# Kernel tuning notes

Hardware: AMD Instinct MI355X
Metric: run time of the kernel (lower is better)

The kernel has to match this reference:

```python
import jax, jax.numpy as jnp
import numpy as np

N_HEAD = 16
N_KV = 4
HEAD_DIM = 128
EPS = float(np.finfo(np.float32).eps)  # torch F.rms_norm default eps


def _rope_tables(T, half, dtype=jnp.float32):
    inv_freq = 1.0 / (10000.0 ** (jnp.arange(half, dtype=dtype) / half))
    ang = jnp.arange(T, dtype=dtype)[:, None] * inv_freq[None, :]  # (T, half)
    cos = jnp.cos(ang)[None, :, None, :]  # (1, T, 1, half)
    sin = jnp.sin(ang)[None, :, None, :]
    return cos, sin


def setup_inputs() -> dict:
    key = jax.random.key(0)
    ks = jax.random.split(key, 5)
    B, T, C = 2, 2048, 2048
    x = jax.random.normal(ks[0], (B, T, C), dtype=jnp.float32)
    cos, sin = _rope_tables(T, HEAD_DIM // 2)
    s = 0.02
    W_Q = jax.random.normal(ks[1], (C, N_HEAD * HEAD_DIM), dtype=jnp.float32) * s
    W_K = jax.random.normal(ks[2], (C, N_KV * HEAD_DIM), dtype=jnp.float32) * s
    W_V = jax.random.normal(ks[3], (C, N_KV * HEAD_DIM), dtype=jnp.float32) * s
    W_O = jax.random.normal(ks[4], (C, C), dtype=jnp.float32) * s
    return {"x": x, "cos": cos, "sin": sin, "W_Q": W_Q, "W_K": W_K, "W_V": W_V, "W_O": W_O}


def _apply_rope(x, cos, sin):
    # x: (B,T,H,D); cos/sin: (1,T,1,D/2)
    d = x.shape[-1] // 2
    x1, x2 = x[..., :d], x[..., d:]
    return jnp.concatenate([x1 * cos + x2 * sin, -x1 * sin + x2 * cos], axis=-1)


def _rms_norm(x):
    return x * jax.lax.rsqrt(jnp.mean(x * x, axis=-1, keepdims=True) + EPS)


def reference(x, cos, sin, W_Q, W_K, W_V, W_O):
    B, T, C = x.shape
    G = N_HEAD // N_KV  # kv groups
    q = (x @ W_Q).reshape(B, T, N_HEAD, HEAD_DIM)
    k = (x @ W_K).reshape(B, T, N_KV, HEAD_DIM)
    v = (x @ W_V).reshape(B, T, N_KV, HEAD_DIM)
    q = _rms_norm(_apply_rope(q, cos[:, :T], sin[:, :T]))
    k = _rms_norm(_apply_rope(k, cos[:, :T], sin[:, :T]))
    # GQA: avoid materializing expanded K/V; group q by kv head
    qg = q.reshape(B, T, N_KV, G, HEAD_DIM)
    scale = 1.0 / jnp.sqrt(jnp.asarray(HEAD_DIM, dtype=x.dtype))
    scores = jnp.einsum("btkgd,bskd->bkgts", qg, k) * scale  # (B,Kv,G,T,T)
    causal = jnp.tril(jnp.ones((T, T), dtype=bool))
    scores = jnp.where(causal, scores, jnp.asarray(-jnp.inf, dtype=scores.dtype))
    attn = jax.nn.softmax(scores, axis=-1)
    out = jnp.einsum("bkgts,bskd->btkgd", attn, v).reshape(B, T, C)
    return out @ W_O
```

## Files before the change

kernel.cpp:

```cpp
#include <hip/hip_runtime.h>
#include <hip/hip_bf16.h>
#include <stdint.h>

typedef __bf16 bf16_4 __attribute__((ext_vector_type(4)));
typedef __bf16 bf16_8 __attribute__((ext_vector_type(8)));
typedef float f32x4 __attribute__((ext_vector_type(4)));

#define AS1 __attribute__((address_space(1)))
#define AS3 __attribute__((address_space(3)))

__device__ __forceinline__ void gload_lds16(const void* g, void* l) {
  __builtin_amdgcn_global_load_lds((const AS1 void*)g, (AS3 void*)l, 16, 0, 0);
}

__global__ void detect_dtype(const void* __restrict__ cosT, int* __restrict__ flag) {
  uint32_t w = *reinterpret_cast<const uint32_t*>(cosT);
  *flag = ((w & 0xFFFFu) == 0x3F80u) ? 1 : 0;
}

__global__ __launch_bounds__(256) void to_bf16_vec(const void* __restrict__ src,
                                                   __bf16* __restrict__ dst,
                                                   int n8, const int* __restrict__ flag) {
  const int i = blockIdx.x * 256 + threadIdx.x;
  if (i >= n8) return;
  if (*flag) {
    reinterpret_cast<int4*>(dst)[i] = reinterpret_cast<const int4*>(src)[i];
  } else {
    const float4* s = reinterpret_cast<const float4*>(src);
    const float4 a = s[2 * i], b = s[2 * i + 1];
    __bf16 o[8] = {(__bf16)a.x, (__bf16)a.y, (__bf16)a.z, (__bf16)a.w,
                   (__bf16)b.x, (__bf16)b.y, (__bf16)b.z, (__bf16)b.w};
    reinterpret_cast<int4*>(dst)[i] = *reinterpret_cast<int4*>(o);
  }
}

__global__ __launch_bounds__(256) void tables_to_f32(const void* __restrict__ c,
                                                     const void* __restrict__ s,
                                                     float* __restrict__ dst, int n,
                                                     const int* __restrict__ flag) {
  const int i = blockIdx.x * 256 + threadIdx.x;
  if (i >= n) return;
  if (*flag) {
    dst[i]     = (float)reinterpret_cast<const __bf16*>(c)[i];
    dst[n + i] = (float)reinterpret_cast<const __bf16*>(s)[i];
  } else {
    dst[i]     = reinterpret_cast<const float*>(c)[i];
    dst[n + i] = reinterpret_cast<const float*>(s)[i];
  }
}

__global__ void transpose_all(const void* __restrict__ WQ, const void* __restrict__ WK,
                              const void* __restrict__ WV, const void* __restrict__ WO,
                              __bf16* __restrict__ Wt, __bf16* __restrict__ WOt,
                              const int* __restrict__ flag) {
  __shared__ __bf16 t[32][33];
  const int bx = blockIdx.x;
  const void* src;
  __bf16* dst;
  int C, c0;
  if (bx < 64)      { src = WQ; dst = Wt;                          C = 2048; c0 = bx * 32; }
  else if (bx < 80) { src = WK; dst = Wt + (size_t)2048 * 2048;    C = 512;  c0 = (bx - 64) * 32; }
  else if (bx < 96) { src = WV; dst = Wt + (size_t)2560 * 2048;    C = 512;  c0 = (bx - 80) * 32; }
  else              { src = WO; dst = WOt;                         C = 2048; c0 = (bx - 96) * 32; }
  const int r0 = blockIdx.y * 32;
  const bool isb = (*flag != 0);
  #pragma unroll
  for (int i = 0; i < 32; i += 8) {
    const size_t idx = (size_t)(r0 + threadIdx.y + i) * C + c0 + threadIdx.x;
    t[threadIdx.y + i][threadIdx.x] =
        isb ? reinterpret_cast<const __bf16*>(src)[idx]
            : (__bf16)reinterpret_cast<const float*>(src)[idx];
  }
  __syncthreads();
  #pragma unroll
  for (int i = 0; i < 32; i += 8)
    dst[(size_t)(c0 + threadIdx.y + i) * 2048 + r0 + threadIdx.x] = t[threadIdx.x][threadIdx.y + i];
}

__global__ void vtrans(const __bf16* __restrict__ qkv, __bf16* __restrict__ vt) {
  __shared__ __bf16 t[32][33];
  const int b = blockIdx.z;
  const int t0 = blockIdx.x * 32, c0 = blockIdx.y * 32;
  #pragma unroll
  for (int i = 0; i < 32; i += 8)
    t[threadIdx.y + i][threadIdx.x] =
        qkv[(size_t)(b * 2048 + t0 + threadIdx.y + i) * 3072 + 2560 + c0 + threadIdx.x];
  __syncthreads();
  #pragma unroll
  for (int i = 0; i < 32; i += 8)
    vt[(size_t)(b * 512 + c0 + threadIdx.y + i) * 2048 + t0 + threadIdx.x] =
        t[threadIdx.x][threadIdx.y + i];
}

template <int DYN>
__global__ __launch_bounds__(512) void gemm8p(const __bf16* __restrict__ A,
                                              const __bf16* __restrict__ Bt,
                                              void* __restrict__ Cv,
                                              int M, int N, int K,
                                              const int* __restrict__ flag) {
  __shared__ __attribute__((aligned(16))) __bf16 As[2][128 * 64];
  __shared__ __attribute__((aligned(16))) __bf16 Bs[2][256 * 64];
  const int tid = threadIdx.x;
  const int lane = tid & 63, w = tid >> 6;
  const int wm = w >> 2, wn = w & 3;
  const int r = lane & 15, g = lane >> 4;
  const int bm = blockIdx.x * 128, bn = blockIdx.y * 256;
  const bool isb = DYN ? (*flag != 0) : true;
  const int NT = K >> 6;

  f32x4 acc[4][4] = {};

#define STA(kt, p, j)                                                              \
  {                                                                                \
    const int o_ = tid * 16 + (j) * 8192;                                          \
    const int row_ = o_ >> 7, blk_ = (o_ >> 4) & 7;                                \
    gload_lds16(A + (size_t)(bm + row_) * K + (kt) * 64 + ((blk_ ^ (row_ & 7)) << 3), \
                (char*)As[p] + o_);                                                \
  }
#define STB(kt, p, j)                                                              \
  {                                                                                \
    const int o_ = tid * 16 + (j) * 8192;                                          \
    const int rl_ = o_ >> 7, blk_ = (o_ >> 4) & 7;                                 \
    const int gr_ = ((rl_ >> 5) & 3) * 64 + ((rl_ >> 7) & 1) * 32 + (rl_ & 31);    \
    gload_lds16(Bt + (size_t)(bn + gr_) * K + (kt) * 64 + ((blk_ ^ (rl_ & 7)) << 3), \
                (char*)Bs[p] + o_);                                                \
  }

  STA(0, 0, 0); STA(0, 0, 1);
  STB(0, 0, 0); STB(0, 0, 1); STB(0, 0, 2); STB(0, 0, 3);
  asm volatile("s_waitcnt vmcnt(2)\ns_barrier" ::: "memory");

  for (int kt = 0; kt < NT; ++kt) {
    const int cur = kt & 1, nxt = cur ^ 1;
    const bool pf = (kt + 1 < NT);
    const char* Ac = (const char*)As[cur];
    const char* Bc = (const char*)Bs[cur];

    bf16_8 af[4][2], bf[2][2];
    #pragma unroll
    for (int m = 0; m < 4; ++m)
      #pragma unroll
      for (int kk = 0; kk < 2; ++kk) {
        const int row = wm * 64 + m * 16 + r;
        af[m][kk] = *reinterpret_cast<const bf16_8*>(
            Ac + row * 128 + (((kk * 4 + g) ^ (row & 7)) << 4));
      }
    #pragma unroll
    for (int n = 0; n < 2; ++n)
      #pragma unroll
      for (int kk = 0; kk < 2; ++kk) {
        const int rl = wn * 32 + n * 16 + r;
        bf[n][kk] = *reinterpret_cast<const bf16_8*>(
            Bc + rl * 128 + (((kk * 4 + g) ^ (rl & 7)) << 4));
      }
    if (pf) { STA(kt + 1, nxt, 0); STA(kt + 1, nxt, 1); STB(kt + 1, nxt, 0); }
    __builtin_amdgcn_s_barrier();
    __builtin_amdgcn_s_setprio(1);
    #pragma unroll
    for (int kk = 0; kk < 2; ++kk)
      #pragma unroll
      for (int m = 0; m < 4; ++m)
        #pragma unroll
        for (int n = 0; n < 2; ++n)
          acc[m][n] = __builtin_amdgcn_mfma_f32_16x16x32_bf16(af[m][kk], bf[n][kk], acc[m][n], 0, 0, 0);
    __builtin_amdgcn_s_setprio(0);
    if (pf) asm volatile("s_waitcnt vmcnt(3)\ns_barrier" ::: "memory");
    else    asm volatile("s_waitcnt vmcnt(0)\ns_barrier" ::: "memory");

    bf16_8 bg[2][2];
    #pragma unroll
    for (int n = 0; n < 2; ++n)
      #pragma unroll
      for (int kk = 0; kk < 2; ++kk) {
        const int rl = 128 + wn * 32 + n * 16 + r;
        bg[n][kk] = *reinterpret_cast<const bf16_8*>(
            Bc + rl * 128 + (((kk * 4 + g) ^ (rl & 7)) << 4));
      }
    if (pf) { STB(kt + 1, nxt, 1); STB(kt + 1, nxt, 2); STB(kt + 1, nxt, 3); }
    __builtin_amdgcn_s_barrier();
    __builtin_amdgcn_s_setprio(1);
    #pragma unroll
    for (int kk = 0; kk < 2; ++kk)
      #pragma unroll
      for (int m = 0; m < 4; ++m)
        #pragma unroll
        for (int n = 0; n < 2; ++n)
          acc[m][n + 2] = __builtin_amdgcn_mfma_f32_16x16x32_bf16(af[m][kk], bg[n][kk], acc[m][n + 2], 0, 0, 0);
    __builtin_amdgcn_s_setprio(0);
    if (pf) asm volatile("s_waitcnt vmcnt(2)\ns_barrier" ::: "memory");
    else    asm volatile("s_waitcnt vmcnt(0)\ns_barrier" ::: "memory");
  }
#undef STA
#undef STB

  #pragma unroll
  for (int m = 0; m < 4; ++m)
    #pragma unroll
    for (int n = 0; n < 4; ++n)
      #pragma unroll
      for (int j = 0; j < 4; ++j) {
        const int row = bm + wm * 64 + m * 16 + g * 4 + j;
        const int col = bn + wn * 64 + n * 16 + r;
        const float v = acc[m][n][j];
        if (isb) reinterpret_cast<__bf16*>(Cv)[(size_t)row * N + col] = (__bf16)v;
        else     reinterpret_cast<float*>(Cv)[(size_t)row * N + col] = v;
      }
}

__global__ __launch_bounds__(256) void rope_rms(__bf16* __restrict__ qkv,
                                                const float* __restrict__ csF) {
  const int gw = blockIdx.x * 4 + (threadIdx.x >> 6);
  const int lane = threadIdx.x & 63;
  const int head = gw % 20;
  const int m = gw / 20;
  const int t = m & 2047;
  __bf16* p = qkv + (size_t)m * 3072 + head * 128;
  const float x1 = (float)p[lane];
  const float x2 = (float)p[lane + 64];
  const float c = csF[t * 64 + lane];
  const float s = csF[131072 + t * 64 + lane];
  const float y1 = x1 * c + x2 * s;
  const float y2 = x2 * c - x1 * s;
  float ss = y1 * y1 + y2 * y2;
  #pragma unroll
  for (int mk = 32; mk >= 1; mk >>= 1) ss += __shfl_xor(ss, mk, 64);
  const float inv = rsqrtf(ss * (1.0f / 128.0f) + 1.1920929e-7f);
  p[lane] = (__bf16)(y1 * inv);
  p[lane + 64] = (__bf16)(y2 * inv);
}

__global__ __launch_bounds__(256) void attn_fwd4(const __bf16* __restrict__ qkv,
                                                 const __bf16* __restrict__ vt,
                                                 __bf16* __restrict__ out) {
  __shared__ __attribute__((aligned(16))) __bf16 Kl[2][64 * 128];
  __shared__ __attribute__((aligned(16))) __bf16 Vl[2][128 * 64];
  __shared__ __attribute__((aligned(16))) __bf16 Pl[4][16][72];

  const int tid = threadIdx.x, lane = tid & 63, w = tid >> 6;
  const int r = lane & 15, g = lane >> 4;
  const int lid = blockIdx.x;
  const int grp = lid & 7, inner = lid >> 3;
  const int b = grp >> 2, kvh = grp & 3;
  const int h = kvh * 4 + (inner & 3);
  const int x = inner >> 2;
  const int qtA = x, qtB = 31 - x;
  const int nA = qtA + 1, nB = qtB + 1;
  const __bf16* Kbase = qkv + (size_t)(b * 2048) * 3072 + 2048 + kvh * 128;
  const __bf16* Vbase = vt + (size_t)((b * 4 + kvh) * 128) * 2048;
  const float sc2 = 0.08838834764831845f * 1.44269504f;

#define STAGE(kt, p)                                                            \
  {                                                                             \
    _Pragma("unroll")                                                           \
    for (int i_ = 0; i_ < 4; ++i_) {                                            \
      const int o_ = tid * 16 + i_ * 4096;                                      \
      const int krow_ = o_ >> 8;                                                \
      const int jj_ = (o_ >> 4) & 15;                                           \
      const int gj_ = (jj_ & 8) | ((jj_ ^ krow_) & 7);                          \
      gload_lds16(Kbase + (size_t)((kt) * 64 + krow_) * 3072 + gj_ * 8,         \
                  (char*)Kl[p] + o_);                                           \
      const int d_ = o_ >> 7;                                                   \
      const int j2_ = (o_ >> 4) & 7;                                            \
      const int g2_ = j2_ ^ (d_ & 7);                                           \
      gload_lds16(Vbase + (size_t)d_ * 2048 + (kt) * 64 + g2_ * 8,              \
                  (char*)Vl[p] + o_);                                           \
    }                                                                           \
  }

#define TILE(qt_, qf_, acc_, mst_, lst_)                                        \
  do {                                                                          \
    f32x4 sacc[4] = {};                                                         \
    _Pragma("unroll")                                                           \
    for (int kb = 0; kb < 4; ++kb) {                                            \
      const int jj = kb * 4 + g;                                                \
      const int jp = (jj & 8) | ((jj ^ (r & 7)) & 7);                           \
      _Pragma("unroll")                                                         \
      for (int n = 0; n < 4; ++n) {                                             \
        const bf16_8 kf = *reinterpret_cast<const bf16_8*>(Kc + (n * 16 + r) * 256 + jp * 16); \
        sacc[n] = __builtin_amdgcn_mfma_f32_16x16x32_bf16(kf, qf_[kb], sacc[n], 0, 0, 0); \
      }                                                                         \
    }                                                                           \
    float p[4][4];                                                              \
    float pm = -1e30f;                                                          \
    _Pragma("unroll")                                                           \
    for (int n = 0; n < 4; ++n)                                                 \
      _Pragma("unroll")                                                         \
      for (int j = 0; j < 4; ++j) {                                             \
        float s = sacc[n][j] * sc2;                                             \
        p[n][j] = s;                                                            \
        pm = fmaxf(pm, s);                                                      \
      }                                                                         \
    if (kt == (qt_)) {                                                          \
      const int qpos_ = (qt_) * 64 + w * 16 + r;                                \
      pm = -1e30f;                                                              \
      _Pragma("unroll")                                                         \
      for (int n = 0; n < 4; ++n)                                               \
        _Pragma("unroll")                                                       \
        for (int j = 0; j < 4; ++j) {                                           \
          if (kt * 64 + n * 16 + g * 4 + j > qpos_) p[n][j] = -1e30f;           \
          pm = fmaxf(pm, p[n][j]);                                              \
        }                                                                       \
    }                                                                           \
    pm = fmaxf(pm, __shfl_xor(pm, 16, 64));                                     \
    pm = fmaxf(pm, __shfl_xor(pm, 32, 64));                                     \
    float mn = mst_;                                                            \
    if (!__all(pm - mst_ <= 12.0f)) {                                           \
      mn = fmaxf(mst_, pm);                                                     \
      const float alpha = exp2f(mst_ - mn);                                     \
      mst_ = mn;                                                                \
      lst_ *= alpha;                                                            \
      float av[4];                                                              \
      _Pragma("unroll")                                                         \
      for (int j = 0; j < 4; ++j) av[j] = __shfl(alpha, g * 4 + j, 64);         \
      _Pragma("unroll")                                                         \
      for (int dt = 0; dt < 8; ++dt)                                            \
        _Pragma("unroll")                                                       \
        for (int j = 0; j < 4; ++j) acc_[dt][j] *= av[j];                       \
    }                                                                           \
    float rs = 0.0f;                                                            \
    _Pragma("unroll")                                                           \
    for (int n = 0; n < 4; ++n)                                                 \
      _Pragma("unroll")                                                         \
      for (int j = 0; j < 4; ++j) {                                             \
        p[n][j] = exp2f(p[n][j] - mn);                                          \
        rs += p[n][j];                                                          \
      }                                                                         \
    rs += __shfl_xor(rs, 16, 64);                                               \
    rs += __shfl_xor(rs, 32, 64);                                               \
    lst_ += rs;                                                                 \
    _Pragma("unroll")                                                           \
    for (int n = 0; n < 4; ++n) {                                               \
      bf16_4 pk;                                                                \
      _Pragma("unroll")                                                         \
      for (int j = 0; j < 4; ++j) pk[j] = (__bf16)p[n][j];                      \
      *reinterpret_cast<bf16_4*>(&Pl[w][r][n * 16 + g * 4]) = pk;               \
    }                                                                           \
    _Pragma("unroll")                                                           \
    for (int half = 0; half < 2; ++half) {                                      \
      const bf16_8 pa = *reinterpret_cast<const bf16_8*>(&Pl[w][r][half * 32 + g * 8]); \
      _Pragma("unroll")                                                         \
      for (int dt = 0; dt < 8; ++dt) {                                          \
        const int d = dt * 16 + r;                                              \
        const bf16_8 vf = *reinterpret_cast<const bf16_8*>(Vc + d * 128 + ((half * 4 + g) ^ (d & 7)) * 16); \
        acc_[dt] = __builtin_amdgcn_mfma_f32_16x16x32_bf16(pa, vf, acc_[dt], 0, 0, 0); \
      }                                                                         \
    }                                                                           \
  } while (0)

  bf16_8 qfA[4], qfB[4];
  {
    const __bf16* qpA = qkv + (size_t)(b * 2048 + qtA * 64 + w * 16 + r) * 3072 + h * 128 + g * 8;
    const __bf16* qpB = qkv + (size_t)(b * 2048 + qtB * 64 + w * 16 + r) * 3072 + h * 128 + g * 8;
    #pragma unroll
    for (int kb = 0; kb < 4; ++kb) {
      qfA[kb] = *reinterpret_cast<const bf16_8*>(qpA + kb * 32);
      qfB[kb] = *reinterpret_cast<const bf16_8*>(qpB + kb * 32);
    }
  }

  f32x4 accA[8] = {}, accB[8] = {};
  float mstA = -1e30f, lstA = 0.0f, mstB = -1e30f, lstB = 0.0f;

  STAGE(0, 0);
  asm volatile("s_waitcnt vmcnt(0)" ::: "memory");
  __syncthreads();

  for (int kt = 0; kt < nB; ++kt) {
    const int cur = kt & 1;
    if (kt + 1 < nB) STAGE(kt + 1, cur ^ 1);
    const char* Kc = (const char*)Kl[cur];
    const char* Vc = (const char*)Vl[cur];

    if (kt < nA) TILE(qtA, qfA, accA, mstA, lstA);
    TILE(qtB, qfB, accB, mstB, lstB);

    asm volatile("s_waitcnt vmcnt(0)" ::: "memory");
    __syncthreads();
  }

  {
    float lv[4];
    #pragma unroll
    for (int j = 0; j < 4; ++j) lv[j] = 1.0f / __shfl(lstA, g * 4 + j, 64);
    #pragma unroll
    for (int dt = 0; dt < 8; ++dt)
      #pragma unroll
      for (int j = 0; j < 4; ++j) {
        const int t = qtA * 64 + w * 16 + g * 4 + j;
        out[(size_t)(b * 2048 + t) * 2048 + h * 128 + dt * 16 + r] = (__bf16)(accA[dt][j] * lv[j]);
      }
  }
  {
    float lv[4];
    #pragma unroll
    for (int j = 0; j < 4; ++j) lv[j] = 1.0f / __shfl(lstB, g * 4 + j, 64);
    #pragma unroll
    for (int dt = 0; dt < 8; ++dt)
      #pragma unroll
      for (int j = 0; j < 4; ++j) {
        const int t = qtB * 64 + w * 16 + g * 4 + j;
        out[(size_t)(b * 2048 + t) * 2048 + h * 128 + dt * 16 + r] = (__bf16)(accB[dt][j] * lv[j]);
      }
  }
#undef STAGE
#undef TILE
}

extern "C" void kernel_launch(void* const* d_in, const int* in_sizes, int n_in,
                              void* d_out, int out_size, void* d_ws, size_t ws_size,
                              hipStream_t stream) {
  const void* x    = d_in[0];
  const void* cosT = d_in[1];
  const void* sinT = d_in[2];
  const void* W_Q  = d_in[3];
  const void* W_K  = d_in[4];
  const void* W_V  = d_in[5];
  const void* W_O  = d_in[6];

  const int B = 2, T = 2048, C = 2048;
  const int M = B * T;
  const int NQKV = 3072;

  char* ws = (char*)d_ws;
  int*    flag = (int*)ws;                       ws += 256;
  float*  csF  = (float*)ws;                     ws += (size_t)2 * 131072 * 4;
  __bf16* xb   = (__bf16*)ws;                    ws += (size_t)M * C * 2;
  __bf16* Wt   = (__bf16*)ws;                    ws += (size_t)NQKV * C * 2;
  __bf16* WOt  = (__bf16*)ws;                    ws += (size_t)C * C * 2;
  __bf16* QKV  = (__bf16*)ws;                    ws += (size_t)M * NQKV * 2;
  __bf16* AO   = (__bf16*)ws;                    ws += (size_t)M * C * 2;
  __bf16* VT   = xb;

  detect_dtype<<<1, 1, 0, stream>>>(cosT, flag);
  tables_to_f32<<<131072 / 256, 256, 0, stream>>>(cosT, sinT, csF, 131072, flag);
  to_bf16_vec<<<(M * C / 8) / 256, 256, 0, stream>>>(x, xb, M * C / 8, flag);

  transpose_all<<<dim3(160, 64), dim3(32, 8), 0, stream>>>(W_Q, W_K, W_V, W_O, Wt, WOt, flag);

  gemm8p<0><<<dim3(M / 128, NQKV / 256), 512, 0, stream>>>(xb, Wt, QKV, M, NQKV, C, flag);
  rope_rms<<<dim3(M * 20 / 4), 256, 0, stream>>>(QKV, csF);
  vtrans<<<dim3(T / 32, 512 / 32, B), dim3(32, 8), 0, stream>>>(QKV, VT);
  attn_fwd4<<<dim3(512), 256, 0, stream>>>(QKV, VT, AO);
  gemm8p<1><<<dim3(M / 128, C / 256), 512, 0, stream>>>(AO, WOt, d_out, M, C, C, flag);
}
```

Before: 230.0 us.

## Single-buffer attention LDS, fold softmax scale into Q, swizzle P tile

The attention kernel drops K/V double buffering to halve LDS use and adds a launch bound of 4 blocks per SM for higher occupancy. Each iteration now loads the tile and waits before computing, so global-load prefetch no longer overlaps compute. The softmax scale times log2(e) is folded into the Q normalization in rope_rms, which removes a multiply per score. The P staging buffer goes from padded rows to an XOR-swizzled layout to avoid bank conflicts while shrinking LDS further.

```diff
diff --git a/kernel.cpp b/kernel.cpp
--- a/kernel.cpp
+++ b/kernel.cpp
@@ -224,17 +224,18 @@
   float ss = y1 * y1 + y2 * y2;
   #pragma unroll
   for (int mk = 32; mk >= 1; mk >>= 1) ss += __shfl_xor(ss, mk, 64);
-  const float inv = rsqrtf(ss * (1.0f / 128.0f) + 1.1920929e-7f);
+  float inv = rsqrtf(ss * (1.0f / 128.0f) + 1.1920929e-7f);
+  if (head < 16) inv *= 0.12751743f;
   p[lane] = (__bf16)(y1 * inv);
   p[lane + 64] = (__bf16)(y2 * inv);
 }
 
-__global__ __launch_bounds__(256) void attn_fwd4(const __bf16* __restrict__ qkv,
-                                                 const __bf16* __restrict__ vt,
-                                                 __bf16* __restrict__ out) {
-  __shared__ __attribute__((aligned(16))) __bf16 Kl[2][64 * 128];
-  __shared__ __attribute__((aligned(16))) __bf16 Vl[2][128 * 64];
-  __shared__ __attribute__((aligned(16))) __bf16 Pl[4][16][72];
+__global__ __launch_bounds__(256, 4) void attn_fwd5(const __bf16* __restrict__ qkv,
+                                                    const __bf16* __restrict__ vt,
+                                                    __bf16* __restrict__ out) {
+  __shared__ __attribute__((aligned(16))) __bf16 Kl[64 * 128];
+  __shared__ __attribute__((aligned(16))) __bf16 Vl[128 * 64];
+  __shared__ __attribute__((aligned(16))) __bf16 Pl[4][16][64];
 
   const int tid = threadIdx.x, lane = tid & 63, w = tid >> 6;
   const int r = lane & 15, g = lane >> 4;
@@ -247,9 +248,8 @@
   const int nA = qtA + 1, nB = qtB + 1;
   const __bf16* Kbase = qkv + (size_t)(b * 2048) * 3072 + 2048 + kvh * 128;
   const __bf16* Vbase = vt + (size_t)((b * 4 + kvh) * 128) * 2048;
-  const float sc2 = 0.08838834764831845f * 1.44269504f;
-
-#define STAGE(kt, p)                                                            \
+
+#define STAGE(kt)                                                               \
   {                                                                             \
     _Pragma("unroll")                                                           \
     for (int i_ = 0; i_ < 4; ++i_) {                                            \
@@ -258,12 +258,12 @@
       const int jj_ = (o_ >> 4) & 15;                                           \
       const int gj_ = (jj_ & 8) | ((jj_ ^ krow_) & 7);                          \
       gload_lds16(Kbase + (size_t)((kt) * 64 + krow_) * 3072 + gj_ * 8,         \
-                  (char*)Kl[p] + o_);                                           \
+                  (char*)Kl + o_);                                              \
       const int d_ = o_ >> 7;                                                   \
       const int j2_ = (o_ >> 4) & 7;                                            \
       const int g2_ = j2_ ^ (d_ & 7);                                           \
       gload_lds16(Vbase + (size_t)d_ * 2048 + (kt) * 64 + g2_ * 8,              \
-                  (char*)Vl[p] + o_);                                           \
+                  (char*)Vl + o_);                                              \
     }                                                                           \
   }
 
@@ -276,7 +276,7 @@
       const int jp = (jj & 8) | ((jj ^ (r & 7)) & 7);                           \
       _Pragma("unroll")                                                         \
       for (int n = 0; n < 4; ++n) {                                             \
-        const bf16_8 kf = *reinterpret_cast<const bf16_8*>(Kc + (n * 16 + r) * 256 + jp * 16); \
+        const bf16_8 kf = *reinterpret_cast<const bf16_8*>((char*)Kl + (n * 16 + r) * 256 + jp * 16); \
         sacc[n] = __builtin_amdgcn_mfma_f32_16x16x32_bf16(kf, qf_[kb], sacc[n], 0, 0, 0); \
       }                                                                         \
     }                                                                           \
@@ -286,7 +286,7 @@
     for (int n = 0; n < 4; ++n)                                                 \
       _Pragma("unroll")                                                         \
       for (int j = 0; j < 4; ++j) {                                             \
-        float s = sacc[n][j] * sc2;                                             \
+        float s = sacc[n][j];                                                   \
         p[n][j] = s;                                                            \
         pm = fmaxf(pm, s);                                                      \
       }                                                                         \
@@ -328,20 +328,24 @@
     rs += __shfl_xor(rs, 16, 64);                                               \
     rs += __shfl_xor(rs, 32, 64);                                               \
     lst_ += rs;                                                                 \
+         \
     _Pragma("unroll")                                                           \
     for (int n = 0; n < 4; ++n) {                                               \
       bf16_4 pk;                                                                \
       _Pragma("unroll")                                                         \
       for (int j = 0; j < 4; ++j) pk[j] = (__bf16)p[n][j];                      \
-      *reinterpret_cast<bf16_4*>(&Pl[w][r][n * 16 + g * 4]) = pk;               \
+      const int blk_ = 2 * n + (g >> 1);                                        \
+      char* pw = (char*)Pl + w * 2048 + r * 128 + ((blk_ ^ (r & 7)) << 4) + (g & 1) * 8; \
+      *reinterpret_cast<bf16_4*>(pw) = pk;                                      \
     }                                                                           \
     _Pragma("unroll")                                                           \
     for (int half = 0; half < 2; ++half) {                                      \
-      const bf16_8 pa = *reinterpret_cast<const bf16_8*>(&Pl[w][r][half * 32 + g * 8]); \
+      const bf16_8 pa = *reinterpret_cast<const bf16_8*>(                       \
+          (char*)Pl + w * 2048 + r * 128 + (((half * 4 + g) ^ (r & 7)) << 4));  \
       _Pragma("unroll")                                                         \
       for (int dt = 0; dt < 8; ++dt) {                                          \
         const int d = dt * 16 + r;                                              \
-        const bf16_8 vf = *reinterpret_cast<const bf16_8*>(Vc + d * 128 + ((half * 4 + g) ^ (d & 7)) * 16); \
+        const bf16_8 vf = *reinterpret_cast<const bf16_8*>((char*)Vl + d * 128 + ((half * 4 + g) ^ (d & 7)) * 16); \
         acc_[dt] = __builtin_amdgcn_mfma_f32_16x16x32_bf16(pa, vf, acc_[dt], 0, 0, 0); \
       }                                                                         \
     }                                                                           \
@@ -361,20 +365,14 @@
   f32x4 accA[8] = {}, accB[8] = {};
   float mstA = -1e30f, lstA = 0.0f, mstB = -1e30f, lstB = 0.0f;
 
-  STAGE(0, 0);
-  asm volatile("s_waitcnt vmcnt(0)" ::: "memory");
-  __syncthreads();
-
   for (int kt = 0; kt < nB; ++kt) {
-    const int cur = kt & 1;
-    if (kt + 1 < nB) STAGE(kt + 1, cur ^ 1);
-    const char* Kc = (const char*)Kl[cur];
-    const char* Vc = (const char*)Vl[cur];
+    STAGE(kt);
+    asm volatile("s_waitcnt vmcnt(0)" ::: "memory");
+    __syncthreads();
 
     if (kt < nA) TILE(qtA, qfA, accA, mstA, lstA);
     TILE(qtB, qfB, accB, mstB, lstB);
 
-    asm volatile("s_waitcnt vmcnt(0)" ::: "memory");
     __syncthreads();
   }
 
@@ -440,6 +438,6 @@
   gemm8p<0><<<dim3(M / 128, NQKV / 256), 512, 0, stream>>>(xb, Wt, QKV, M, NQKV, C, flag);
   rope_rms<<<dim3(M * 20 / 4), 256, 0, stream>>>(QKV, csF);
   vtrans<<<dim3(T / 32, 512 / 32, B), dim3(32, 8), 0, stream>>>(QKV, VT);
-  attn_fwd4<<<dim3(512), 256, 0, stream>>>(QKV, VT, AO);
+  attn_fwd5<<<dim3(512), 256, 0, stream>>>(QKV, VT, AO);
   gemm8p<1><<<dim3(M / 128, C / 256), 512, 0, stream>>>(AO, WOt, d_out, M, C, C, flag);
 }
```

New measurement: 326.3 us. 1.42x slower.
